# Optimization experiments

Measured on AMD Instinct MI355X. Metric: run time of the kernel, lower is better.

Reference implementation:

```python
import jax, jax.numpy as jnp
import numpy as np

D_MODEL = 256
N_LAYER = 4
D_INNER = 512   # expand=2
D_STATE = 16
DT_RANK = 16    # ceil(d_model/16)
D_CONV = 4
VOCAB = 16
BATCH = 1
SEQLEN = 4096
EPS = 1e-5


def setup_inputs() -> dict:
    key = jax.random.key(0)
    ks = jax.random.split(key, 10)
    s = 0.02
    A_init = jnp.log(jnp.arange(1, D_STATE + 1, dtype=jnp.float32))  # S4D-real init
    return {
        "input_ids": jax.random.randint(ks[0], (BATCH, SEQLEN), 0, VOCAB, dtype=jnp.int32),
        "embed_w": jax.random.normal(ks[1], (VOCAB, D_MODEL), jnp.float32) * s,
        "norm_w": jnp.ones((N_LAYER, D_MODEL), jnp.float32),
        "in_proj_w": jax.random.normal(ks[2], (N_LAYER, 2 * D_INNER, D_MODEL), jnp.float32) * s,
        "out_proj_w": jax.random.normal(ks[3], (N_LAYER, D_MODEL, D_INNER), jnp.float32) * s,
        "conv_w": jax.random.normal(ks[4], (N_LAYER, 2, D_INNER, D_CONV), jnp.float32) * s,
        "conv_b": jnp.zeros((N_LAYER, 2, D_INNER), jnp.float32),
        "x_proj_w": jax.random.normal(ks[5], (N_LAYER, 2, DT_RANK + 2 * D_STATE, D_INNER), jnp.float32) * s,
        "dt_proj_w": jax.random.normal(ks[6], (N_LAYER, 2, D_INNER, DT_RANK), jnp.float32) * s,
        "dt_proj_b": jax.random.normal(ks[7], (N_LAYER, 2, D_INNER), jnp.float32) * 0.1,
        "A_log": jnp.broadcast_to(A_init, (N_LAYER, 2, D_INNER, D_STATE)) + 0.0,
        "Dp": jnp.ones((N_LAYER, 2, D_INNER), jnp.float32),
        "norm_f_w": jnp.ones((D_MODEL,), jnp.float32),
    }


def rmsnorm(x, w):
    return x * jax.lax.rsqrt(jnp.mean(x * x, axis=-1, keepdims=True) + EPS) * w


def selective_scan(u, dt, A, Bm, Cm, Dv):
    # u, dt: (B,L,Di); A: (Di,N); Bm, Cm: (B,L,N); Dv: (Di,)
    dA = jnp.exp(dt[..., None] * A)                         # (B,L,Di,N)
    dBu = dt[..., None] * Bm[:, :, None, :] * u[..., None]  # (B,L,Di,N)

    def step(h, xs):
        dA_t, dBu_t, C_t = xs
        h = dA_t * h + dBu_t                                # (B,Di,N)
        y = jnp.einsum('bdn,bn->bd', h, C_t)
        return h, y

    h0 = jnp.zeros((u.shape[0], D_INNER, D_STATE), u.dtype)
    xs = (jnp.moveaxis(dA, 1, 0), jnp.moveaxis(dBu, 1, 0), jnp.moveaxis(Cm, 1, 0))
    _, ys = jax.lax.scan(step, h0, xs)                      # (L,B,Di)
    return jnp.moveaxis(ys, 0, 1) + u * Dv


def mamba_dir(x, in_w, out_w, cw, cb, xpw, dtw, dtb, a_log, dv):
    # x: (B,L,D)
    xz = jnp.einsum('bld,ed->ble', x, in_w)                 # (B,L,2*Di)
    u, z = jnp.split(xz, 2, axis=-1)
    # causal depthwise conv1d
    uc = jnp.moveaxis(u, 1, 2)                              # (B,Di,L)
    uc = jax.lax.conv_general_dilated(
        uc, cw[:, None, :], (1,), [(D_CONV - 1, 0)],
        feature_group_count=D_INNER, dimension_numbers=('NCH', 'OIH', 'NCH'))
    u = jax.nn.silu(jnp.moveaxis(uc, 1, 2) + cb)            # (B,L,Di)
    xdb = jnp.einsum('bld,ed->ble', u, xpw)                 # (B,L,dt_rank+2N)
    dt_r, Bm, Cm = jnp.split(xdb, [DT_RANK, DT_RANK + D_STATE], axis=-1)
    dt = jax.nn.softplus(jnp.einsum('blr,dr->bld', dt_r, dtw) + dtb)
    A = -jnp.exp(a_log)                                     # (Di,N)
    y = selective_scan(u, dt, A, Bm, Cm, dv)
    y = y * jax.nn.silu(z)
    return jnp.einsum('bld,od->blo', y, out_w)


def reference(input_ids, embed_w, norm_w, in_proj_w, out_proj_w, conv_w, conv_b,
              x_proj_w, dt_proj_w, dt_proj_b, A_log, Dp, norm_f_w):
    h = embed_w[input_ids]                                  # (B,L,D)
    residual = None
    for i in range(N_LAYER):
        residual = h if residual is None else h + residual  # residual_in_fp32
        hn = rmsnorm(residual, norm_w[i])
        out_f = mamba_dir(hn, in_proj_w[i], out_proj_w[i], conv_w[i, 0], conv_b[i, 0],
                          x_proj_w[i, 0], dt_proj_w[i, 0], dt_proj_b[i, 0], A_log[i, 0], Dp[i, 0])
        out_r = mamba_dir(hn[:, ::-1], in_proj_w[i], out_proj_w[i], conv_w[i, 1], conv_b[i, 1],
                          x_proj_w[i, 1], dt_proj_w[i, 1], dt_proj_b[i, 1], A_log[i, 1], Dp[i, 1])[:, ::-1]
        h = out_f + out_r                                   # bidirectional 'add'
    residual = h + residual
    return rmsnorm(residual, norm_f_w)
```

## Files before the change

### kernel.cpp

```cpp
#include <hip/hip_runtime.h>
#include <hip/hip_bf16.h>
#include <math.h>

#define L_  4096
#define D_  256
#define DI_ 512
#define NS_ 16
#define NC_ 128
#define CH_ 32

typedef __attribute__((ext_vector_type(8))) short short8;
typedef __attribute__((ext_vector_type(4))) short short4v;
typedef __attribute__((ext_vector_type(4))) float f32x4;

__global__ __launch_bounds__(256) void prep_kernel(const int* __restrict__ ids,
    const float* __restrict__ ew, const float* __restrict__ inw,
    const float* __restrict__ outw, const float* __restrict__ xpw,
    float* __restrict__ res, __hip_bfloat16* __restrict__ inw_b,
    __hip_bfloat16* __restrict__ outw_b, __hip_bfloat16* __restrict__ xpw_b) {
  int idx = blockIdx.x * 256 + threadIdx.x;
  int l = idx >> 8, d = idx & 255;
  res[idx] = ew[ids[l] * D_ + d];
  inw_b[idx] = __float2bfloat16(inw[idx]);
  {
    int layer = idx >> 18;
    int rem = idx & 262143;
    int o = rem >> 10, k = rem & 1023;
    outw_b[idx] = __float2bfloat16(outw[((size_t)layer * 256 + o) * 512 + (k & 511)]);
  }
  if (idx < 4 * 2 * 64 * 512) {
    int layer = idx >> 16;
    int rem = idx & 65535;
    int dir = rem >> 15;
    int r = (rem >> 9) & 63, k = idx & 511;
    float v = (r < 48) ? xpw[(((size_t)layer * 2 + dir) * 48 + r) * 512 + k] : 0.f;
    xpw_b[idx] = __float2bfloat16(v);
  }
}

template<bool BF16OUT>
__global__ __launch_bounds__(256) void rmsnorm_kernel(float* __restrict__ residual,
    const float* __restrict__ hadd, const float* __restrict__ w, void* __restrict__ out) {
  int row = blockIdx.x * 4 + (threadIdx.x >> 6);
  int lane = threadIdx.x & 63;
  size_t o = (size_t)row * D_ + lane * 4;
  float4 v = *(const float4*)(residual + o);
  if (hadd) {
    float4 a = *(const float4*)(hadd + o);
    v.x += a.x; v.y += a.y; v.z += a.z; v.w += a.w;
    *(float4*)(residual + o) = v;
  }
  float sq = fmaf(v.x, v.x, fmaf(v.y, v.y, fmaf(v.z, v.z, v.w * v.w)));
  #pragma unroll
  for (int s = 32; s > 0; s >>= 1) sq += __shfl_xor(sq, s, 64);
  float scale = rsqrtf(sq * (1.f / D_) + 1e-5f);
  float4 wv = *(const float4*)(w + lane * 4);
  float r0 = v.x * scale * wv.x, r1 = v.y * scale * wv.y;
  float r2 = v.z * scale * wv.z, r3 = v.w * scale * wv.w;
  if (BF16OUT) {
    __hip_bfloat16* ob = (__hip_bfloat16*)out + o;
    short4v s4;
    s4[0] = __bfloat16_as_short(__float2bfloat16(r0));
    s4[1] = __bfloat16_as_short(__float2bfloat16(r1));
    s4[2] = __bfloat16_as_short(__float2bfloat16(r2));
    s4[3] = __bfloat16_as_short(__float2bfloat16(r3));
    *reinterpret_cast<short4v*>(ob) = s4;
  } else {
    float4 r = {r0, r1, r2, r3};
    *((float4*)out + (o >> 2)) = r;
  }
}

__device__ __forceinline__ void gload_lds16(const void* g, void* l) {
  __builtin_amdgcn_global_load_lds((const __attribute__((address_space(1))) unsigned int*)g,
                                   (__attribute__((address_space(3))) unsigned int*)l,
                                   16, 0, 0);
}

template<int BM, int BN, bool BF16OUT>
__global__ __launch_bounds__(256) void gemm_bt_bf16(const __hip_bfloat16* __restrict__ A,
    const __hip_bfloat16* __restrict__ B, void* __restrict__ Cv, int M, int N, int K,
    size_t sA, size_t sB, size_t sC) {
  A += (size_t)blockIdx.z * sA; B += (size_t)blockIdx.z * sB;
  constexpr int FM = (BM / 2) / 16, FN = (BN / 2) / 16;
  constexpr int ABYTES = BM * 64, BBYTES = BN * 64;
  __shared__ __attribute__((aligned(16))) char As[ABYTES];
  __shared__ __attribute__((aligned(16))) char Bs[BBYTES];
  int tid = threadIdx.x, lane = tid & 63, w = tid >> 6;
  int bm = blockIdx.y * BM, bn = blockIdx.x * BN;
  int wr = (w >> 1) * (BM / 2), wc = (w & 1) * (BN / 2);
  f32x4 acc[FM][FN] = {};
  for (int k0 = 0; k0 < K; k0 += 32) {
    __syncthreads();
    #pragma unroll
    for (int i = 0; i < ABYTES / 4096; ++i) {
      int x = (i * 256 + tid) * 16;
      int xs = x ^ (((x >> 7) & 3) << 4);
      int row = xs >> 6, col = (xs & 63) >> 1;
      gload_lds16(A + (size_t)(bm + row) * K + k0 + col, As + i * 4096 + w * 1024);
    }
    #pragma unroll
    for (int i = 0; i < BBYTES / 4096; ++i) {
      int x = (i * 256 + tid) * 16;
      int xs = x ^ (((x >> 7) & 3) << 4);
      int row = xs >> 6, col = (xs & 63) >> 1;
      gload_lds16(B + (size_t)(bn + row) * K + k0 + col, Bs + i * 4096 + w * 1024);
    }
    __syncthreads();
    short8 af[FM], bf[FN];
    #pragma unroll
    for (int m = 0; m < FM; ++m) {
      int row = wr + m * 16 + (lane & 15);
      int x = row * 64 + ((lane >> 4) * 16);
      x ^= ((x >> 7) & 3) << 4;
      af[m] = *reinterpret_cast<const short8*>(As + x);
    }
    #pragma unroll
    for (int n = 0; n < FN; ++n) {
      int row = wc + n * 16 + (lane & 15);
      int x = row * 64 + ((lane >> 4) * 16);
      x ^= ((x >> 7) & 3) << 4;
      bf[n] = *reinterpret_cast<const short8*>(Bs + x);
    }
    #pragma unroll
    for (int m = 0; m < FM; ++m)
      #pragma unroll
      for (int n = 0; n < FN; ++n)
        acc[m][n] = __builtin_amdgcn_mfma_f32_16x16x32_bf16(af[m], bf[n], acc[m][n], 0, 0, 0);
  }
  #pragma unroll
  for (int m = 0; m < FM; ++m)
    #pragma unroll
    for (int n = 0; n < FN; ++n)
      #pragma unroll
      for (int j = 0; j < 4; ++j) {
        size_t off = (size_t)blockIdx.z * sC +
                     (size_t)(bm + wr + m * 16 + (lane >> 4) * 4 + j) * N + bn + wc + n * 16 + (lane & 15);
        if (BF16OUT) ((__hip_bfloat16*)Cv)[off] = __float2bfloat16(acc[m][n][j]);
        else         ((float*)Cv)[off] = acc[m][n][j];
      }
}

__global__ __launch_bounds__(256) void xproj_conv(const __hip_bfloat16* __restrict__ xz,
    const float* __restrict__ cw, const float* __restrict__ cb,
    const __hip_bfloat16* __restrict__ xpw_b, float* __restrict__ xdb,
    __hip_bfloat16* __restrict__ ucb) {
  int dir = blockIdx.y;
  int l0 = blockIdx.x * 32;
  int tid = threadIdx.x, lane = tid & 63, w = tid >> 6;
  __shared__ __attribute__((aligned(16))) unsigned short sxz[36][512];
  __shared__ __attribute__((aligned(16))) unsigned short su[32][520];
  __shared__ __attribute__((aligned(16))) char Bs[4096];
  #pragma unroll
  for (int it = 0; it < 9; ++it) {
    int s = it * 4 + w;
    int sc = s > 34 ? 34 : s;
    int f = l0 - 3 + sc;
    int row = dir ? (L_ - 1 - f) : f;
    row = row < 0 ? 0 : (row > L_ - 1 ? L_ - 1 : row);
    gload_lds16((const char*)xz + (size_t)row * 2048 + lane * 16, (char*)sxz + s * 1024);
  }
  __syncthreads();
  unsigned short* ucs = (unsigned short*)ucb;
  #pragma unroll
  for (int half = 0; half < 2; ++half) {
    int ch = half * 256 + tid;
    float4 wv = *(const float4*)(cw + ((size_t)dir * DI_ + ch) * 4);
    float bias = cb[(size_t)dir * DI_ + ch];
    #pragma unroll 4
    for (int t = 0; t < 32; ++t) {
      float acc = bias;
      #pragma unroll
      for (int k = 0; k < 4; ++k) {
        float xv = (l0 == 0 && t + k < 3) ? 0.f
                 : __uint_as_float((unsigned)sxz[t + k][ch] << 16);
        acc = fmaf(((const float*)&wv)[k], xv, acc);
      }
      float uvf = acc * __builtin_amdgcn_rcpf(1.f + __expf(-acc));
      unsigned short bits = (unsigned short)__bfloat16_as_short(__float2bfloat16(uvf));
      su[t][ch] = bits;
      ucs[((size_t)dir * L_ + l0 + t) * DI_ + ch] = bits;
    }
  }
  const __hip_bfloat16* B = xpw_b + (size_t)dir * 64 * 512;
  int wr = (w >> 1) * 16, wc = (w & 1) * 32;
  f32x4 acc2[2] = {};
  for (int k0 = 0; k0 < 512; k0 += 32) {
    __syncthreads();
    {
      int x = tid * 16;
      int xs = x ^ (((x >> 7) & 3) << 4);
      int row = xs >> 6, col = (xs & 63) >> 1;
      gload_lds16(B + (size_t)row * 512 + k0 + col, Bs + w * 1024);
    }
    __syncthreads();
    short8 af = *reinterpret_cast<const short8*>(
        (const char*)su + (wr + (lane & 15)) * 1040 + (k0 + (lane >> 4) * 8) * 2);
    #pragma unroll
    for (int n = 0; n < 2; ++n) {
      int row = wc + n * 16 + (lane & 15);
      int x = row * 64 + ((lane >> 4) * 16);
      x ^= ((x >> 7) & 3) << 4;
      short8 bf8 = *reinterpret_cast<const short8*>(Bs + x);
      acc2[n] = __builtin_amdgcn_mfma_f32_16x16x32_bf16(af, bf8, acc2[n], 0, 0, 0);
    }
  }
  #pragma unroll
  for (int n = 0; n < 2; ++n)
    #pragma unroll
    for (int j = 0; j < 4; ++j)
      xdb[((size_t)dir * L_ + l0 + wr + (lane >> 4) * 4 + j) * 64 + wc + n * 16 + (lane & 15)]
          = acc2[n][j];
}

__device__ __forceinline__ void scan_stage3(int tid, int lane, int w, int q, int dir, int c,
    const float* __restrict__ xdb, const __hip_bfloat16* __restrict__ uc,
    const float* __restrict__ dtw, const float* __restrict__ dtbp,
    float (*sxdb)[64], unsigned short (*su)[128], float (*sdt)[128]) {
  const char* bg = (const char*)(xdb + ((size_t)dir * L_ + (size_t)c * CH_) * 64);
  const char* ug = (const char*)(uc + ((size_t)dir * L_ + (size_t)c * CH_) * DI_ + q * 128);
  #pragma unroll
  for (int i = 0; i < 2; ++i)
    gload_lds16(bg + w * 2048 + i * 1024 + lane * 16, (char*)sxdb + w * 2048 + i * 1024);
  #pragma unroll
  for (int i = 0; i < 2; ++i) {
    int byte = (w * 128 + i * 64 + lane) * 16;
    gload_lds16(ug + (byte >> 8) * 1024 + (byte & 255), (char*)su + w * 2048 + i * 1024);
  }
  __syncthreads();
  int dlx = tid & 127, tst = tid >> 7;
  int dc = q * 128 + dlx;
  const float4* wr = (const float4*)(dtw + ((size_t)dir * DI_ + dc) * 16);
  float4 w0 = wr[0], w1 = wr[1], w2 = wr[2], w3 = wr[3];
  float bias = dtbp[(size_t)dir * DI_ + dc];
  #pragma unroll
  for (int i = 0; i < 16; ++i) {
    int t = tst + i * 2;
    const float4* xr = (const float4*)&sxdb[t][0];
    float4 x0 = xr[0], x1 = xr[1], x2 = xr[2], x3 = xr[3];
    float acc = bias;
    acc = fmaf(w0.x, x0.x, fmaf(w0.y, x0.y, fmaf(w0.z, x0.z, fmaf(w0.w, x0.w, acc))));
    acc = fmaf(w1.x, x1.x, fmaf(w1.y, x1.y, fmaf(w1.z, x1.z, fmaf(w1.w, x1.w, acc))));
    acc = fmaf(w2.x, x2.x, fmaf(w2.y, x2.y, fmaf(w2.z, x2.z, fmaf(w2.w, x2.w, acc))));
    acc = fmaf(w3.x, x3.x, fmaf(w3.y, x3.y, fmaf(w3.z, x3.z, fmaf(w3.w, x3.w, acc))));
    float e = __expf(fminf(acc, 20.f));
    sdt[t][dlx] = acc > 20.f ? acc : __logf(1.f + e);
  }
  __syncthreads();
}

__global__ __launch_bounds__(256) void scan_pass1(const __hip_bfloat16* __restrict__ uc,
    const float* __restrict__ xdb, const float* __restrict__ dtw,
    const float* __restrict__ dtbp, const float* __restrict__ A_log,
    float* __restrict__ Pb, float* __restrict__ Qb) {
  int dir = blockIdx.y;
  int c = blockIdx.x >> 2, q = blockIdx.x & 3;
  int tid = threadIdx.x, lane = tid & 63, w = tid >> 6;
  int dl = tid >> 1, nh = tid & 1;
  int d = q * 128 + dl;
  __shared__ __attribute__((aligned(16))) float sxdb[CH_][64];
  __shared__ __attribute__((aligned(16))) unsigned short su[CH_][128];
  __shared__ __attribute__((aligned(16))) float sdt[CH_][128];
  float Av[8], P[8], Q[8];
  const float4* Ab4 = (const float4*)(A_log + ((size_t)dir * DI_ + d) * 16 + nh * 8);
  float4 a0 = Ab4[0], a1 = Ab4[1];
  float al[8] = {a0.x, a0.y, a0.z, a0.w, a1.x, a1.y, a1.z, a1.w};
  #pragma unroll
  for (int j = 0; j < 8; ++j) { Av[j] = -__expf(al[j]); P[j] = 1.f; Q[j] = 0.f; }
  scan_stage3(tid, lane, w, q, dir, c, xdb, uc, dtw, dtbp, sxdb, su, sdt);
  #pragma unroll 8
  for (int t = 0; t < CH_; ++t) {
    float dtv = sdt[t][dl];
    float uv  = __uint_as_float((unsigned)su[t][dl] << 16);
    float du = dtv * uv;
    const float4* Br = (const float4*)&sxdb[t][16 + nh * 8];
    float4 b0 = Br[0], b1 = Br[1];
    float bb[8] = {b0.x, b0.y, b0.z, b0.w, b1.x, b1.y, b1.z, b1.w};
    #pragma unroll
    for (int j = 0; j < 8; ++j) {
      float dA = __expf(dtv * Av[j]);
      P[j] *= dA;
      Q[j] = fmaf(dA, Q[j], bb[j] * du);
    }
  }
  size_t ob = ((size_t)dir * NC_ + c) * 8192 + (size_t)(nh * 8) * 512 + d;
  #pragma unroll
  for (int j = 0; j < 8; ++j) { Pb[ob + j * 512] = P[j]; Qb[ob + j * 512] = Q[j]; }
}

__global__ __launch_bounds__(256) void combine_a(const float* __restrict__ Pb,
    const float* __restrict__ Qb, float* __restrict__ Pseg, float* __restrict__ Qseg) {
  int chain = blockIdx.x * 256 + threadIdx.x;
  int seg = blockIdx.y;
  int dir = chain >> 13, s = chain & 8191;
  size_t base = (size_t)dir * NC_ * 8192 + s;
  float P = 1.f, Q = 0.f;
  #pragma unroll 16
  for (int cc = 0; cc < 16; ++cc) {
    size_t o = base + (size_t)(seg * 16 + cc) * 8192;
    float p = Pb[o], q = Qb[o];
    Q = fmaf(p, Q, q);
    P *= p;
  }
  Pseg[seg * 16384 + chain] = P;
  Qseg[seg * 16384 + chain] = Q;
}

__global__ __launch_bounds__(256) void combine_c(const float* __restrict__ Pb,
    const float* __restrict__ Qb, const float* __restrict__ Pseg,
    const float* __restrict__ Qseg, float* __restrict__ H0) {
  int chain = blockIdx.x * 256 + threadIdx.x;
  int seg = blockIdx.y;
  int dir = chain >> 13, s = chain & 8191;
  size_t base = (size_t)dir * NC_ * 8192 + s;
  float h = 0.f;
  for (int s2 = 0; s2 < seg; ++s2)
    h = fmaf(Pseg[s2 * 16384 + chain], h, Qseg[s2 * 16384 + chain]);
  #pragma unroll 16
  for (int cc = 0; cc < 16; ++cc) {
    size_t o = base + (size_t)(seg * 16 + cc) * 8192;
    H0[o] = h;
    h = fmaf(Pb[o], h, Qb[o]);
  }
}

__global__ __launch_bounds__(256) void scan_pass2(const __hip_bfloat16* __restrict__ uc,
    const float* __restrict__ xdb, const float* __restrict__ dtw,
    const float* __restrict__ dtbp, const float* __restrict__ A_log,
    const float* __restrict__ Dp, const __hip_bfloat16* __restrict__ xz,
    const float* __restrict__ H0, __hip_bfloat16* __restrict__ yg) {
  int dir = blockIdx.y;
  int c = blockIdx.x >> 2, q = blockIdx.x & 3;
  int tid = threadIdx.x, lane = tid & 63, w = tid >> 6;
  int dl = tid >> 1, nh = tid & 1;
  int d = q * 128 + dl;
  __shared__ __attribute__((aligned(16))) float sxdb[CH_][64];
  __shared__ __attribute__((aligned(16))) unsigned short su[CH_][128];
  __shared__ __attribute__((aligned(16))) float sdt[CH_][128];
  float Av[8], h[8];
  const float4* Ab4 = (const float4*)(A_log + ((size_t)dir * DI_ + d) * 16 + nh * 8);
  float4 a0 = Ab4[0], a1 = Ab4[1];
  float al[8] = {a0.x, a0.y, a0.z, a0.w, a1.x, a1.y, a1.z, a1.w};
  size_t ob = ((size_t)dir * NC_ + c) * 8192 + (size_t)(nh * 8) * 512 + d;
  #pragma unroll
  for (int j = 0; j < 8; ++j) { Av[j] = -__expf(al[j]); h[j] = H0[ob + j * 512]; }
  float Dv = Dp[(size_t)dir * DI_ + d];
  scan_stage3(tid, lane, w, q, dir, c, xdb, uc, dtw, dtbp, sxdb, su, sdt);
  #pragma unroll 8
  for (int t = 0; t < CH_; ++t) {
    float dtv = sdt[t][dl];
    float uv  = __uint_as_float((unsigned)su[t][dl] << 16);
    float du = dtv * uv;
    const float4* Br = (const float4*)&sxdb[t][16 + nh * 8];
    const float4* Cr = (const float4*)&sxdb[t][32 + nh * 8];
    float4 b0 = Br[0], b1 = Br[1], c0 = Cr[0], c1 = Cr[1];
    float bb[8] = {b0.x, b0.y, b0.z, b0.w, b1.x, b1.y, b1.z, b1.w};
    float cc[8] = {c0.x, c0.y, c0.z, c0.w, c1.x, c1.y, c1.z, c1.w};
    float y = 0.f;
    #pragma unroll
    for (int j = 0; j < 8; ++j) {
      float dA = __expf(dtv * Av[j]);
      h[j] = fmaf(dA, h[j], bb[j] * du);
      y = fmaf(h[j], cc[j], y);
    }
    y += __shfl_xor(y, 1, 64);
    if (nh == 0) {
      int l = c * CH_ + t;
      int pos = dir ? (L_ - 1 - l) : l;
      float zv = __bfloat162float(xz[(size_t)pos * 1024 + DI_ + d]);
      float g = zv * __builtin_amdgcn_rcpf(1.f + __expf(-zv));
      yg[(size_t)pos * 1024 + (size_t)dir * DI_ + d] = __float2bfloat16((y + uv * Dv) * g);
    }
  }
}

extern "C" void kernel_launch(void* const* d_in, const int* in_sizes, int n_in,
                              void* d_out, int out_size, void* d_ws, size_t ws_size,
                              hipStream_t stream) {
  const int*   ids       = (const int*)  d_in[0];
  const float* embed_w   = (const float*)d_in[1];
  const float* norm_w    = (const float*)d_in[2];
  const float* in_proj_w = (const float*)d_in[3];
  const float* out_proj_w= (const float*)d_in[4];
  const float* conv_w    = (const float*)d_in[5];
  const float* conv_b    = (const float*)d_in[6];
  const float* x_proj_w  = (const float*)d_in[7];
  const float* dt_proj_w = (const float*)d_in[8];
  const float* dt_proj_b = (const float*)d_in[9];
  const float* A_log     = (const float*)d_in[10];
  const float* Dp        = (const float*)d_in[11];
  const float* norm_f_w  = (const float*)d_in[12];

  float* ws = (float*)d_ws;
  float* residual = ws; ws += (size_t)L_ * D_;
  float* xdb      = ws; ws += (size_t)2 * L_ * 64;
  float* hbuf     = ws; ws += (size_t)L_ * D_;
  float* Pb       = ws; ws += (size_t)2 * NC_ * 8192;
  float* Qb       = ws; ws += (size_t)2 * NC_ * 8192;
  float* H0       = ws; ws += (size_t)2 * NC_ * 8192;
  float* Pseg     = ws; ws += (size_t)8 * 16384;
  float* Qseg     = ws; ws += (size_t)8 * 16384;
  __hip_bfloat16* hn_b   = (__hip_bfloat16*)ws;
  __hip_bfloat16* xz_b   = hn_b + (size_t)L_ * D_;
  __hip_bfloat16* yg_b   = xz_b + (size_t)L_ * 1024;
  __hip_bfloat16* uc_b   = yg_b + (size_t)L_ * 1024;
  __hip_bfloat16* inw_b  = uc_b + (size_t)2 * L_ * DI_;
  __hip_bfloat16* outw_b = inw_b + (size_t)4 * 1024 * D_;
  __hip_bfloat16* xpw_b  = outw_b + (size_t)4 * D_ * 1024;

  prep_kernel<<<L_ * D_ / 256, 256, 0, stream>>>(ids, embed_w, in_proj_w, out_proj_w,
                                                 x_proj_w, residual, inw_b, outw_b, xpw_b);

  for (int i = 0; i < 4; ++i) {
    rmsnorm_kernel<true><<<L_ / 4, 256, 0, stream>>>(residual, i ? hbuf : nullptr,
                                                     norm_w + (size_t)i * D_, hn_b);
    gemm_bt_bf16<128, 64, true><<<dim3(1024 / 64, L_ / 128, 1), 256, 0, stream>>>(
        hn_b, inw_b + (size_t)i * 1024 * D_, xz_b, L_, 1024, D_, 0, 0, 0);
    xproj_conv<<<dim3(L_ / 32, 2), 256, 0, stream>>>(
        xz_b, conv_w + (size_t)i * 2 * DI_ * 4, conv_b + (size_t)i * 2 * DI_,
        xpw_b + (size_t)i * 2 * 64 * DI_, xdb, uc_b);
    dim3 gsc(NC_ * 4, 2);
    scan_pass1<<<gsc, 256, 0, stream>>>(
        uc_b, xdb, dt_proj_w + (size_t)i * 2 * DI_ * 16, dt_proj_b + (size_t)i * 2 * DI_,
        A_log + (size_t)i * 2 * DI_ * NS_, Pb, Qb);
    combine_a<<<dim3(64, 8), 256, 0, stream>>>(Pb, Qb, Pseg, Qseg);
    combine_c<<<dim3(64, 8), 256, 0, stream>>>(Pb, Qb, Pseg, Qseg, H0);
    scan_pass2<<<gsc, 256, 0, stream>>>(
        uc_b, xdb, dt_proj_w + (size_t)i * 2 * DI_ * 16, dt_proj_b + (size_t)i * 2 * DI_,
        A_log + (size_t)i * 2 * DI_ * NS_, Dp + (size_t)i * 2 * DI_,
        xz_b, H0, yg_b);
    gemm_bt_bf16<64, 64, false><<<dim3(D_ / 64, L_ / 64, 1), 256, 0, stream>>>(
        yg_b, outw_b + (size_t)i * D_ * 1024, hbuf, L_, D_, 1024, 0, 0, 0);
  }

  rmsnorm_kernel<false><<<L_ / 4, 256, 0, stream>>>(residual, hbuf, norm_f_w, d_out);
}
```

Baseline: 437.3 us.

## Fuse chunk-local scan pass into xproj_conv kernel using on-chip conv and xproj results

Merges the first scan pass (per-chunk P/Q products) into the x-projection/conv kernel, reusing the conv output and projected dt/B values already held in shared memory instead of relaunching and reloading them from global memory. Each thread now handles a full channel with all 16 states over two halves, computing the dt projection and softplus inline. This removes one kernel launch and one global reload of xdb/uc, but cuts parallelism from 1024 blocks to 256 blocks per layer, raises register pressure (16-wide P/Q arrays) and uses more shared memory.

```diff
diff --git a/kernel.cpp b/kernel.cpp
--- a/kernel.cpp
+++ b/kernel.cpp
@@ -141,16 +141,19 @@
       }
 }
 
-__global__ __launch_bounds__(256) void xproj_conv(const __hip_bfloat16* __restrict__ xz,
+__global__ __launch_bounds__(256) void xproj_conv_scan(const __hip_bfloat16* __restrict__ xz,
     const float* __restrict__ cw, const float* __restrict__ cb,
-    const __hip_bfloat16* __restrict__ xpw_b, float* __restrict__ xdb,
-    __hip_bfloat16* __restrict__ ucb) {
+    const __hip_bfloat16* __restrict__ xpw_b, const float* __restrict__ dtw,
+    const float* __restrict__ dtbp, const float* __restrict__ A_log,
+    float* __restrict__ xdb, __hip_bfloat16* __restrict__ ucb,
+    float* __restrict__ Pb, float* __restrict__ Qb) {
   int dir = blockIdx.y;
   int l0 = blockIdx.x * 32;
   int tid = threadIdx.x, lane = tid & 63, w = tid >> 6;
   __shared__ __attribute__((aligned(16))) unsigned short sxz[36][512];
   __shared__ __attribute__((aligned(16))) unsigned short su[32][520];
   __shared__ __attribute__((aligned(16))) char Bs[4096];
+  __shared__ __attribute__((aligned(16))) float sxdb[32][64];
   #pragma unroll
   for (int it = 0; it < 9; ++it) {
     int s = it * 4 + w;
@@ -208,9 +211,59 @@
   #pragma unroll
   for (int n = 0; n < 2; ++n)
     #pragma unroll
-    for (int j = 0; j < 4; ++j)
-      xdb[((size_t)dir * L_ + l0 + wr + (lane >> 4) * 4 + j) * 64 + wc + n * 16 + (lane & 15)]
-          = acc2[n][j];
+    for (int j = 0; j < 4; ++j) {
+      int tt = wr + (lane >> 4) * 4 + j;
+      int col = wc + n * 16 + (lane & 15);
+      xdb[((size_t)dir * L_ + l0 + tt) * 64 + col] = acc2[n][j];
+      sxdb[tt][col] = acc2[n][j];
+    }
+  __syncthreads();
+  size_t pqbase = ((size_t)dir * NC_ + blockIdx.x) * 8192;
+  #pragma unroll
+  for (int half = 0; half < 2; ++half) {
+    int ch = half * 256 + tid;
+    const float4* wr4 = (const float4*)(dtw + ((size_t)dir * DI_ + ch) * 16);
+    float4 w0 = wr4[0], w1 = wr4[1], w2 = wr4[2], w3 = wr4[3];
+    float bias = dtbp[(size_t)dir * DI_ + ch];
+    const float4* Ab4 = (const float4*)(A_log + ((size_t)dir * DI_ + ch) * 16);
+    float4 a0 = Ab4[0], a1 = Ab4[1], a2 = Ab4[2], a3 = Ab4[3];
+    float Av[16] = {a0.x, a0.y, a0.z, a0.w, a1.x, a1.y, a1.z, a1.w,
+                    a2.x, a2.y, a2.z, a2.w, a3.x, a3.y, a3.z, a3.w};
+    #pragma unroll
+    for (int n = 0; n < 16; ++n) Av[n] = -__expf(Av[n]);
+    float P[16], Q[16];
+    #pragma unroll
+    for (int n = 0; n < 16; ++n) { P[n] = 1.f; Q[n] = 0.f; }
+    #pragma unroll 2
+    for (int t = 0; t < 32; ++t) {
+      const float4* xr = (const float4*)&sxdb[t][0];
+      float4 x0 = xr[0], x1 = xr[1], x2 = xr[2], x3 = xr[3];
+      float accd = bias;
+      accd = fmaf(w0.x, x0.x, fmaf(w0.y, x0.y, fmaf(w0.z, x0.z, fmaf(w0.w, x0.w, accd))));
+      accd = fmaf(w1.x, x1.x, fmaf(w1.y, x1.y, fmaf(w1.z, x1.z, fmaf(w1.w, x1.w, accd))));
+      accd = fmaf(w2.x, x2.x, fmaf(w2.y, x2.y, fmaf(w2.z, x2.z, fmaf(w2.w, x2.w, accd))));
+      accd = fmaf(w3.x, x3.x, fmaf(w3.y, x3.y, fmaf(w3.z, x3.z, fmaf(w3.w, x3.w, accd))));
+      float e = __expf(fminf(accd, 20.f));
+      float dtv = accd > 20.f ? accd : __logf(1.f + e);
+      float uv = __uint_as_float((unsigned)su[t][ch] << 16);
+      float du = dtv * uv;
+      const float4* Br4 = (const float4*)&sxdb[t][16];
+      float4 B0 = Br4[0], B1 = Br4[1], B2 = Br4[2], B3 = Br4[3];
+      float bb[16] = {B0.x, B0.y, B0.z, B0.w, B1.x, B1.y, B1.z, B1.w,
+                      B2.x, B2.y, B2.z, B2.w, B3.x, B3.y, B3.z, B3.w};
+      #pragma unroll
+      for (int n = 0; n < 16; ++n) {
+        float dA = __expf(dtv * Av[n]);
+        P[n] *= dA;
+        Q[n] = fmaf(dA, Q[n], bb[n] * du);
+      }
+    }
+    #pragma unroll
+    for (int n = 0; n < 16; ++n) {
+      Pb[pqbase + n * 512 + ch] = P[n];
+      Qb[pqbase + n * 512 + ch] = Q[n];
+    }
+  }
 }
 
 __device__ __forceinline__ void scan_stage3(int tid, int lane, int w, int q, int dir, int c,
@@ -247,45 +300,6 @@
     sdt[t][dlx] = acc > 20.f ? acc : __logf(1.f + e);
   }
   __syncthreads();
-}
-
-__global__ __launch_bounds__(256) void scan_pass1(const __hip_bfloat16* __restrict__ uc,
-    const float* __restrict__ xdb, const float* __restrict__ dtw,
-    const float* __restrict__ dtbp, const float* __restrict__ A_log,
-    float* __restrict__ Pb, float* __restrict__ Qb) {
-  int dir = blockIdx.y;
-  int c = blockIdx.x >> 2, q = blockIdx.x & 3;
-  int tid = threadIdx.x, lane = tid & 63, w = tid >> 6;
-  int dl = tid >> 1, nh = tid & 1;
-  int d = q * 128 + dl;
-  __shared__ __attribute__((aligned(16))) float sxdb[CH_][64];
-  __shared__ __attribute__((aligned(16))) unsigned short su[CH_][128];
-  __shared__ __attribute__((aligned(16))) float sdt[CH_][128];
-  float Av[8], P[8], Q[8];
-  const float4* Ab4 = (const float4*)(A_log + ((size_t)dir * DI_ + d) * 16 + nh * 8);
-  float4 a0 = Ab4[0], a1 = Ab4[1];
-  float al[8] = {a0.x, a0.y, a0.z, a0.w, a1.x, a1.y, a1.z, a1.w};
-  #pragma unroll
-  for (int j = 0; j < 8; ++j) { Av[j] = -__expf(al[j]); P[j] = 1.f; Q[j] = 0.f; }
-  scan_stage3(tid, lane, w, q, dir, c, xdb, uc, dtw, dtbp, sxdb, su, sdt);
-  #pragma unroll 8
-  for (int t = 0; t < CH_; ++t) {
-    float dtv = sdt[t][dl];
-    float uv  = __uint_as_float((unsigned)su[t][dl] << 16);
-    float du = dtv * uv;
-    const float4* Br = (const float4*)&sxdb[t][16 + nh * 8];
-    float4 b0 = Br[0], b1 = Br[1];
-    float bb[8] = {b0.x, b0.y, b0.z, b0.w, b1.x, b1.y, b1.z, b1.w};
-    #pragma unroll
-    for (int j = 0; j < 8; ++j) {
-      float dA = __expf(dtv * Av[j]);
-      P[j] *= dA;
-      Q[j] = fmaf(dA, Q[j], bb[j] * du);
-    }
-  }
-  size_t ob = ((size_t)dir * NC_ + c) * 8192 + (size_t)(nh * 8) * 512 + d;
-  #pragma unroll
-  for (int j = 0; j < 8; ++j) { Pb[ob + j * 512] = P[j]; Qb[ob + j * 512] = Q[j]; }
 }
 
 __global__ __launch_bounds__(256) void combine_a(const float* __restrict__ Pb,
@@ -416,16 +430,14 @@
                                                      norm_w + (size_t)i * D_, hn_b);
     gemm_bt_bf16<128, 64, true><<<dim3(1024 / 64, L_ / 128, 1), 256, 0, stream>>>(
         hn_b, inw_b + (size_t)i * 1024 * D_, xz_b, L_, 1024, D_, 0, 0, 0);
-    xproj_conv<<<dim3(L_ / 32, 2), 256, 0, stream>>>(
+    xproj_conv_scan<<<dim3(L_ / 32, 2), 256, 0, stream>>>(
         xz_b, conv_w + (size_t)i * 2 * DI_ * 4, conv_b + (size_t)i * 2 * DI_,
-        xpw_b + (size_t)i * 2 * 64 * DI_, xdb, uc_b);
-    dim3 gsc(NC_ * 4, 2);
-    scan_pass1<<<gsc, 256, 0, stream>>>(
-        uc_b, xdb, dt_proj_w + (size_t)i * 2 * DI_ * 16, dt_proj_b + (size_t)i * 2 * DI_,
-        A_log + (size_t)i * 2 * DI_ * NS_, Pb, Qb);
+        xpw_b + (size_t)i * 2 * 64 * DI_, dt_proj_w + (size_t)i * 2 * DI_ * 16,
+        dt_proj_b + (size_t)i * 2 * DI_, A_log + (size_t)i * 2 * DI_ * NS_,
+        xdb, uc_b, Pb, Qb);
     combine_a<<<dim3(64, 8), 256, 0, stream>>>(Pb, Qb, Pseg, Qseg);
     combine_c<<<dim3(64, 8), 256, 0, stream>>>(Pb, Qb, Pseg, Qseg, H0);
-    scan_pass2<<<gsc, 256, 0, stream>>>(
+    scan_pass2<<<dim3(NC_ * 4, 2), 256, 0, stream>>>(
         uc_b, xdb, dt_proj_w + (size_t)i * 2 * DI_ * 16, dt_proj_b + (size_t)i * 2 * DI_,
         A_log + (size_t)i * 2 * DI_ * NS_, Dp + (size_t)i * 2 * DI_,
         xz_b, H0, yg_b);
```

Result: no change. 431.8 us (-1.3%).
